# Kernel optimization log

Measured on AMD Instinct MI355X. Metric: run time of the kernel, lower is better.

The kernel has to match this reference:

```python
import jax, jax.numpy as jnp
import numpy as np

N, E, DIN, DOUT = 30000, 480000, 512, 512


def setup_inputs() -> dict:
    key = jax.random.key(0)
    ks = jax.random.split(key, 20)
    inp = {}
    inp["x"] = jax.random.normal(ks[0], (N, DIN), jnp.float32)
    inp["edge_index"] = jax.random.randint(ks[1], (2, E), 0, N, dtype=jnp.int64)
    inp["edge_weight"] = jax.random.uniform(ks[2], (E,), jnp.float32)
    sc = 1.0 / np.sqrt(DIN)
    sl = 1.0 / np.sqrt(2 * DOUT)
    for i, g in enumerate(["i", "f", "g", "o"]):
        inp[f"Wc_{g}"] = jax.random.normal(ks[3 + 4 * i], (DIN, DOUT), jnp.float32) * sc
        inp[f"bc_{g}"] = jnp.zeros((DOUT,), jnp.float32)
        inp[f"Wl_{g}"] = jax.random.normal(ks[4 + 4 * i], (2 * DOUT, DOUT), jnp.float32) * sl
        inp[f"bl_{g}"] = jnp.zeros((DOUT,), jnp.float32)
    return inp


def _gcn_norm(src, dst, w, n):
    # add self loops with weight 1.0 (improved=False), then symmetric normalization
    loops = jnp.arange(n, dtype=src.dtype)
    src = jnp.concatenate([src, loops])
    dst = jnp.concatenate([dst, loops])
    w = jnp.concatenate([w, jnp.ones((n,), w.dtype)])
    deg = jax.ops.segment_sum(w, dst, num_segments=n)
    dinv = jnp.where(deg > 0, jax.lax.rsqrt(jnp.where(deg > 0, deg, 1.0)), 0.0)
    norm = dinv[src] * w * dinv[dst]
    return src, dst, norm


def reference(x, edge_index, edge_weight,
              Wc_i, bc_i, Wl_i, bl_i,
              Wc_f, bc_f, Wl_f, bl_f,
              Wc_g, bc_g, Wl_g, bl_g,
              Wc_o, bc_o, Wl_o, bl_o):
    n = x.shape[0]
    src, dst, norm = _gcn_norm(edge_index[0], edge_index[1], edge_weight, n)
    H = jnp.zeros((n, DOUT), x.dtype)  # _set_hidden_state default
    C = jnp.zeros((n, DOUT), x.dtype)  # _set_cell_state default

    def conv(Wc, bc):
        xw = x @ Wc                                        # [N, DOUT] dense GEMM
        agg = jax.ops.segment_sum(norm[:, None] * xw[src], dst, num_segments=n)
        return agg + bc

    def gate(Wc, bc, Wl, bl, act):
        z = jnp.concatenate([conv(Wc, bc), H], axis=1)      # [N, 2*DOUT]
        return act(z @ Wl + bl)

    I = gate(Wc_i, bc_i, Wl_i, bl_i, jax.nn.sigmoid)
    F = gate(Wc_f, bc_f, Wl_f, bl_f, jax.nn.sigmoid)
    G = gate(Wc_g, bc_g, Wl_g, bl_g, jnp.tanh)
    O = gate(Wc_o, bc_o, Wl_o, bl_o, jax.nn.sigmoid)
    Cn = F * C + I * G
    Hn = O * jnp.tanh(Cn)
    return O, Hn, Cn
```

## Files before the change

### kernel.cpp

```cpp
#include <hip/hip_runtime.h>
#include <stdint.h>

typedef __bf16 bf16;
typedef __attribute__((ext_vector_type(4))) float f4;
typedef __attribute__((ext_vector_type(4))) float f32x4;
typedef __attribute__((ext_vector_type(8))) __bf16 bf8v;
typedef __attribute__((ext_vector_type(4))) __bf16 bf4v;

#define NN 30000
#define MPAD 30080
#define OUTSTRIDE 15360000
#define XB 7500
#define SC_B 1875
#define TWO32 4294967296.0

typedef __attribute__((address_space(3))) unsigned int as3_u32;
typedef __attribute__((address_space(1))) unsigned int as1_u32;

__device__ __forceinline__ void gl_lds16(const void* g, void* l) {
  __builtin_amdgcn_global_load_lds((as1_u32*)g, (as3_u32*)l, 16, 0, 0);
}

__global__ void k_xp(const float* __restrict__ x, bf16* __restrict__ xbf,
                     const int* __restrict__ ei, const float* __restrict__ ew,
                     double* __restrict__ degcnt, int E) {
  int b = blockIdx.x;
  if (b < XB) {
    int i = b * 256 + threadIdx.x;
    const f4* x4 = (const f4*)x;
    f4 a = x4[2 * i], c = x4[2 * i + 1];
    bf8v o;
#pragma unroll
    for (int j = 0; j < 4; ++j) { o[j] = (bf16)a[j]; o[4 + j] = (bf16)c[j]; }
    ((bf8v*)xbf)[i] = o;
  } else {
    int e = (b - XB) * 256 + threadIdx.x;
    if (e < E) {
      int d = ei[E + e];
      atomicAdd(&degcnt[d], (double)ew[e] + TWO32);
    }
  }
}

__global__ void k_doffs(const double* __restrict__ degcnt, float* __restrict__ dinv,
                        int* __restrict__ gctr, int2* __restrict__ off2, int n) {
  int i = blockIdx.x * 256 + threadIdx.x;
  if (i >= n) return;
  double v = degcnt[i];
  double c = (double)(long long)(v * (1.0 / TWO32));
  int cnt = (int)c;
  float deg = (float)(v - c * TWO32);
  dinv[i] = rsqrtf(deg + 1.0f);
  int start = atomicAdd(gctr, cnt);
  off2[i] = make_int2(start, start + cnt);
}

__global__ void k_fused(const int* __restrict__ ei, const float* __restrict__ ew,
                        const float* __restrict__ dinv, const int2* __restrict__ off2,
                        int* __restrict__ cursor, int2* __restrict__ sn, int E,
                        const float* __restrict__ WcA, const float* __restrict__ WlA,
                        const float* __restrict__ WcB, const float* __restrict__ WlB,
                        const float* __restrict__ WcC, const float* __restrict__ WlC,
                        bf16* __restrict__ Wt,
                        const float* __restrict__ bcA, const float* __restrict__ blA,
                        const float* __restrict__ bcB, const float* __restrict__ blB,
                        const float* __restrict__ bcC, const float* __restrict__ blC,
                        float* __restrict__ bcomb) {
  __shared__ float sWc[64][17];
  __shared__ float sWl[16][64];
  __shared__ float smr[4][64];
  int b = blockIdx.x;
  if (b < SC_B) {
    int e = b * 256 + threadIdx.x;
    if (e >= E) return;
    int s = ei[e], d = ei[E + e];
    int pos = off2[d].x + atomicAdd(&cursor[d], 1);
    sn[pos] = make_int2(s, __float_as_int(dinv[s] * ew[e] * dinv[d]));
  } else if (b < SC_B + 192) {
    int bb = b - SC_B;
    int g = bb >> 6, rem = bb & 63;
    const float* Wc; const float* Wl;
    if (g == 0)      { Wc = WcA; Wl = WlA; }
    else if (g == 1) { Wc = WcB; Wl = WlB; }
    else             { Wc = WcC; Wl = WlC; }
    int k0 = (rem & 7) * 64, j0 = (rem >> 3) * 64;
    int t = threadIdx.x, tx = t & 15, ty = t >> 4;
    float acc[4][4] = {};
    for (int c0 = 0; c0 < 512; c0 += 16) {
      { int kk = t >> 2, c4 = (t & 3) * 4;
        f4 v = *(const f4*)(Wc + (size_t)(k0 + kk) * 512 + c0 + c4);
#pragma unroll
        for (int j = 0; j < 4; ++j) sWc[kk][c4 + j] = v[j]; }
      { int cc = t >> 4, j4 = (t & 15) * 4;
        f4 v = *(const f4*)(Wl + (size_t)(c0 + cc) * 512 + j0 + j4);
        *(f4*)&sWl[cc][j4] = v; }
      __syncthreads();
#pragma unroll
      for (int cc = 0; cc < 16; ++cc) {
        float wcv[4], wlv[4];
#pragma unroll
        for (int q = 0; q < 4; ++q) wcv[q] = sWc[tx * 4 + q][cc];
#pragma unroll
        for (int a = 0; a < 4; ++a) wlv[a] = sWl[cc][ty * 4 + a];
#pragma unroll
        for (int a = 0; a < 4; ++a)
#pragma unroll
          for (int q = 0; q < 4; ++q) acc[a][q] += wlv[a] * wcv[q];
      }
      __syncthreads();
    }
#pragma unroll
    for (int a = 0; a < 4; ++a) {
      bf4v o;
#pragma unroll
      for (int q = 0; q < 4; ++q) o[q] = (bf16)acc[a][q];
      *(bf4v*)&Wt[((size_t)g * 512 + j0 + ty * 4 + a) * 512 + k0 + tx * 4] = o;
    }
  } else {
    int bb = b - SC_B - 192;
    int g = bb >> 3, jc = bb & 7;
    const float* bc; const float* bl; const float* Wl;
    if (g == 0)      { bc = bcA; bl = blA; Wl = WlA; }
    else if (g == 1) { bc = bcB; bl = blB; Wl = WlB; }
    else             { bc = bcC; bl = blC; Wl = WlC; }
    int jl = threadIdx.x & 63, part = threadIdx.x >> 6;
    int j = jc * 64 + jl;
    float s = 0.f;
    for (int c = part * 128; c < part * 128 + 128; ++c)
      s += bc[c] * Wl[(size_t)c * 512 + j];
    smr[part][jl] = s;
    __syncthreads();
    if (part == 0)
      bcomb[g * 512 + j] = bl[j] + smr[0][jl] + smr[1][jl] + smr[2][jl] + smr[3][jl];
  }
}

__global__ __launch_bounds__(256) void k_agg(const int2* __restrict__ off2, const int2* __restrict__ sn,
                                             const float* __restrict__ dinv, const bf16* __restrict__ xbf,
                                             bf16* __restrict__ ybf) {
  int wv = (blockIdx.x * 256 + threadIdx.x) >> 6;
  int lane = threadIdx.x & 63;
  if (wv >= MPAD) return;
  bf16* yrow = ybf + ((size_t)wv << 9) + lane * 8;
  if (wv >= NN) {
    bf8v z;
#pragma unroll
    for (int j = 0; j < 8; ++j) z[j] = (bf16)0.f;
    *(bf8v*)yrow = z;
    return;
  }
  float acc[8];
  float s0 = dinv[wv]; s0 *= s0;
  bf8v xv0 = *(const bf8v*)(xbf + ((size_t)wv << 9) + lane * 8);
#pragma unroll
  for (int j = 0; j < 8; ++j) acc[j] = s0 * (float)xv0[j];
  int2 seg = off2[wv];
  int e = seg.x, end = seg.y;
  int2 p0, p1, p2, p3;
  const bool have = (e + 4 <= end);
  if (have) { p0 = sn[e]; p1 = sn[e + 1]; p2 = sn[e + 2]; p3 = sn[e + 3]; }
  for (; e + 8 <= end; e += 4) {
    int2 q0 = sn[e + 4], q1 = sn[e + 5], q2 = sn[e + 6], q3 = sn[e + 7];
    bf8v v0 = *(const bf8v*)(xbf + ((size_t)p0.x << 9) + lane * 8);
    bf8v v1 = *(const bf8v*)(xbf + ((size_t)p1.x << 9) + lane * 8);
    bf8v v2 = *(const bf8v*)(xbf + ((size_t)p2.x << 9) + lane * 8);
    bf8v v3 = *(const bf8v*)(xbf + ((size_t)p3.x << 9) + lane * 8);
    float n0 = __int_as_float(p0.y), n1 = __int_as_float(p1.y);
    float n2 = __int_as_float(p2.y), n3 = __int_as_float(p3.y);
#pragma unroll
    for (int j = 0; j < 8; ++j)
      acc[j] += n0 * (float)v0[j] + n1 * (float)v1[j] + n2 * (float)v2[j] + n3 * (float)v3[j];
    p0 = q0; p1 = q1; p2 = q2; p3 = q3;
  }
  if (have) {
    bf8v v0 = *(const bf8v*)(xbf + ((size_t)p0.x << 9) + lane * 8);
    bf8v v1 = *(const bf8v*)(xbf + ((size_t)p1.x << 9) + lane * 8);
    bf8v v2 = *(const bf8v*)(xbf + ((size_t)p2.x << 9) + lane * 8);
    bf8v v3 = *(const bf8v*)(xbf + ((size_t)p3.x << 9) + lane * 8);
    float n0 = __int_as_float(p0.y), n1 = __int_as_float(p1.y);
    float n2 = __int_as_float(p2.y), n3 = __int_as_float(p3.y);
#pragma unroll
    for (int j = 0; j < 8; ++j)
      acc[j] += n0 * (float)v0[j] + n1 * (float)v1[j] + n2 * (float)v2[j] + n3 * (float)v3[j];
    e += 4;
  }
  for (; e < end; ++e) {
    int2 p = sn[e];
    bf8v v = *(const bf8v*)(xbf + ((size_t)p.x << 9) + lane * 8);
    float nn = __int_as_float(p.y);
#pragma unroll
    for (int j = 0; j < 8; ++j) acc[j] += nn * (float)v[j];
  }
  bf8v o;
#pragma unroll
  for (int j = 0; j < 8; ++j) o[j] = (bf16)acc[j];
  *(bf8v*)yrow = o;
}

__global__ __launch_bounds__(256, 5) void k_gemm(const bf16* __restrict__ A, const bf16* __restrict__ Bt,
                                                 const float* __restrict__ bcomb, float* __restrict__ out) {
  __shared__ __align__(16) char lds[32768];
  const int t = threadIdx.x, lane = t & 63, w = t >> 6;
  const int wm = w >> 1, wn = w & 1;
  const int d = blockIdx.x;
  const int s = (d & 7) * 470 + (d >> 3);
  const int m0 = (s >> 3) * 64, n0 = (s & 7) * 64;
  const int l15 = lane & 15, lhi = lane >> 4;
  f32x4 acc[3][2][2] = {};

  const int lq = lane >> 2;
  const int sw = (lane >> 3) & 3;
  const int kcol = 16 * ((lane & 3) ^ sw);
  const int rswz = 16 * (lhi ^ ((l15 >> 1) & 3));

  const char* aS = (const char*)A + ((size_t)(m0 + w * 16 + lq) << 10) + kcol;
  const char* bS[3];
#pragma unroll
  for (int i = 0; i < 3; ++i) {
    int bi = i * 4 + w, g = bi >> 2, q = bi & 3;
    bS[i] = (const char*)Bt + ((size_t)(g * 512 + n0 + q * 16 + lq) << 10) + kcol;
  }
  const int vA = (wm * 32 + l15) * 64 + rswz;
  const int vB = 4096 + (wn * 32 + l15) * 64 + rswz;

  auto stage = [&](int bufoff, int kp) {
    gl_lds16(aS + kp * 64, lds + bufoff + w * 1024 + lane * 16);
#pragma unroll
    for (int i = 0; i < 3; ++i)
      gl_lds16(bS[i] + kp * 64, lds + bufoff + 4096 + (i * 4 + w) * 1024 + lane * 16);
  };

  auto compute = [&](int bufoff) {
    bf8v af[2];
#pragma unroll
    for (int mi = 0; mi < 2; ++mi)
      af[mi] = *(const bf8v*)(lds + bufoff + vA + mi * 1024);
#pragma unroll
    for (int g = 0; g < 3; ++g) {
      bf8v b0 = *(const bf8v*)(lds + bufoff + vB + g * 4096);
      bf8v b1 = *(const bf8v*)(lds + bufoff + vB + g * 4096 + 1024);
#pragma unroll
      for (int mi = 0; mi < 2; ++mi) {
        acc[g][mi][0] = __builtin_amdgcn_mfma_f32_16x16x32_bf16(b0, af[mi], acc[g][mi][0], 0, 0, 0);
        acc[g][mi][1] = __builtin_amdgcn_mfma_f32_16x16x32_bf16(b1, af[mi], acc[g][mi][1], 0, 0, 0);
      }
    }
  };

  stage(0, 0);
  stage(16384, 1);
#pragma unroll
  for (int kp = 0; kp < 16; ++kp) {
    if (kp < 15) asm volatile("s_waitcnt vmcnt(4)" ::: "memory");
    else         asm volatile("s_waitcnt vmcnt(0)" ::: "memory");
    __builtin_amdgcn_sched_barrier(0);
    __builtin_amdgcn_s_barrier();
    __builtin_amdgcn_sched_barrier(0);
    compute((kp & 1) * 16384);
    __builtin_amdgcn_sched_barrier(0);
    __builtin_amdgcn_s_barrier();
    __builtin_amdgcn_sched_barrier(0);
    if (kp < 14) stage((kp & 1) * 16384, kp + 2);
  }

#pragma unroll
  for (int ni = 0; ni < 2; ++ni) {
    int nb = n0 + wn * 32 + ni * 16 + lhi * 4;
    f4 bI = *(const f4*)&bcomb[nb];
    f4 bG = *(const f4*)&bcomb[512 + nb];
    f4 bO = *(const f4*)&bcomb[1024 + nb];
#pragma unroll
    for (int mi = 0; mi < 2; ++mi) {
      int row = m0 + wm * 32 + mi * 16 + l15;
      if (row < NN) {
        f4 vO, vH, vC;
#pragma unroll
        for (int r = 0; r < 4; ++r) {
          float zi = acc[0][mi][ni][r] + bI[r];
          float zg = acc[1][mi][ni][r] + bG[r];
          float zo = acc[2][mi][ni][r] + bO[r];
          float I = 1.f / (1.f + __expf(-zi));
          float e2g = __expf(2.f * zg);
          float G = (e2g - 1.f) / (e2g + 1.f);
          float O = 1.f / (1.f + __expf(-zo));
          float Cn = I * G;
          float e2c = __expf(2.f * Cn);
          float tc = (e2c - 1.f) / (e2c + 1.f);
          vO[r] = O; vH[r] = O * tc; vC[r] = Cn;
        }
        size_t base = ((size_t)row << 9) + nb;
        __builtin_nontemporal_store(vO, (f4*)&out[base]);
        __builtin_nontemporal_store(vH, (f4*)&out[OUTSTRIDE + base]);
        __builtin_nontemporal_store(vC, (f4*)&out[2 * OUTSTRIDE + base]);
      }
    }
  }
}

extern "C" void kernel_launch(void* const* d_in, const int* in_sizes, int n_in,
                              void* d_out, int out_size, void* d_ws, size_t ws_size,
                              hipStream_t stream) {
  const float* x   = (const float*)d_in[0];
  const int*   ei  = (const int*)d_in[1];
  const float* ew  = (const float*)d_in[2];
  const float* Wc_i = (const float*)d_in[3];
  const float* bc_i = (const float*)d_in[4];
  const float* Wl_i = (const float*)d_in[5];
  const float* bl_i = (const float*)d_in[6];
  const float* Wc_g = (const float*)d_in[11];
  const float* bc_g = (const float*)d_in[12];
  const float* Wl_g = (const float*)d_in[13];
  const float* bl_g = (const float*)d_in[14];
  const float* Wc_o = (const float*)d_in[15];
  const float* bc_o = (const float*)d_in[16];
  const float* Wl_o = (const float*)d_in[17];
  const float* bl_o = (const float*)d_in[18];

  const int E = in_sizes[2];
  const int n = in_sizes[0] / 512;
  const int NB = (n + 255) / 256;

  char* ws = (char*)d_ws;
  bf16*  ybf   = (bf16*)ws;
  float* dinv  = (float*)(ws + 30801920);
  bf16*  Wt    = (bf16*)(ws + 30924800);
  float* bcomb = (float*)(ws + 32497664);
  (void)ws_size;

  char* ob = (char*)d_out;
  float*  out    = (float*)d_out;
  bf16*   xbf    = (bf16*)ob;
  int2*   sn     = (int2*)(ob + 30720000);
  double* degcnt = (double*)(ob + 34560000);
  int*    curs   = (int*)(ob + 34800000);
  int*    gctr   = (int*)(ob + 34920000);
  int2*   off2   = (int2*)(ob + 34920064);
  (void)out_size; (void)n_in;

  hipMemsetAsync(degcnt, 0, 360064, stream);
  k_xp<<<XB + (E + 255) / 256, 256, 0, stream>>>(x, xbf, ei, ew, degcnt, E);
  k_doffs<<<NB, 256, 0, stream>>>(degcnt, dinv, gctr, off2, n);
  k_fused<<<SC_B + 192 + 24, 256, 0, stream>>>(ei, ew, dinv, off2, curs, sn, E,
                                               Wc_i, Wl_i, Wc_g, Wl_g, Wc_o, Wl_o, Wt,
                                               bc_i, bl_i, bc_g, bl_g, bc_o, bl_o, bcomb);
  k_agg<<<(MPAD * 64 + 255) / 256, 256, 0, stream>>>(off2, sn, dinv, xbf, ybf);
  k_gemm<<<3760, 256, 0, stream>>>(ybf, Wt, bcomb, out);
}
```

Measured before the change: 279.1 us.

## Slice features into column panels for cache-local gather, pack edge metadata

Stores bf16 node features and aggregated outputs as 8 column slices of 64 values, so each aggregation pass gathers from a small, cache-resident slice. Each wave processes 8 edges at once, with groups of 8 lanes covering the slice, and combines the partial sums with cross-lane shuffles. Edge metadata is packed into 32 bits: a 16-bit source index plus a bf16-rounded norm. The GEMM A-tile loads are remapped to the sliced layout. The risks are reduced norm precision, a node-count limit of 65536, and shuffle reduction overhead.

```diff
diff --git a/kernel.cpp b/kernel.cpp
--- a/kernel.cpp
+++ b/kernel.cpp
@@ -13,6 +13,8 @@
 #define XB 7500
 #define SC_B 1875
 #define TWO32 4294967296.0
+#define SLE 1925120
+#define SLB 3850240
 
 typedef __attribute__((address_space(3))) unsigned int as3_u32;
 typedef __attribute__((address_space(1))) unsigned int as1_u32;
@@ -21,18 +23,20 @@
   __builtin_amdgcn_global_load_lds((as1_u32*)g, (as3_u32*)l, 16, 0, 0);
 }
 
-__global__ void k_xp(const float* __restrict__ x, bf16* __restrict__ xbf,
+__global__ void k_xp(const float* __restrict__ x, bf16* __restrict__ xs,
                      const int* __restrict__ ei, const float* __restrict__ ew,
                      double* __restrict__ degcnt, int E) {
   int b = blockIdx.x;
   if (b < XB) {
     int i = b * 256 + threadIdx.x;
+    int node = i >> 6, chunk = i & 63;
+    int slice = chunk >> 3, sub = chunk & 7;
     const f4* x4 = (const f4*)x;
     f4 a = x4[2 * i], c = x4[2 * i + 1];
     bf8v o;
 #pragma unroll
     for (int j = 0; j < 4; ++j) { o[j] = (bf16)a[j]; o[4 + j] = (bf16)c[j]; }
-    ((bf8v*)xbf)[i] = o;
+    *(bf8v*)(xs + (size_t)slice * SLE + (size_t)node * 64 + sub * 8) = o;
   } else {
     int e = (b - XB) * 256 + threadIdx.x;
     if (e < E) {
@@ -57,7 +61,7 @@
 
 __global__ void k_fused(const int* __restrict__ ei, const float* __restrict__ ew,
                         const float* __restrict__ dinv, const int2* __restrict__ off2,
-                        int* __restrict__ cursor, int2* __restrict__ sn, int E,
+                        int* __restrict__ cursor, unsigned* __restrict__ sn1, int E,
                         const float* __restrict__ WcA, const float* __restrict__ WlA,
                         const float* __restrict__ WcB, const float* __restrict__ WlB,
                         const float* __restrict__ WcC, const float* __restrict__ WlC,
@@ -75,7 +79,8 @@
     if (e >= E) return;
     int s = ei[e], d = ei[E + e];
     int pos = off2[d].x + atomicAdd(&cursor[d], 1);
-    sn[pos] = make_int2(s, __float_as_int(dinv[s] * ew[e] * dinv[d]));
+    float nrm = dinv[s] * ew[e] * dinv[d];
+    sn1[pos] = ((__float_as_uint(nrm) + 0x8000u) & 0xFFFF0000u) | (unsigned)s;
   } else if (b < SC_B + 192) {
     int bb = b - SC_B;
     int g = bb >> 6, rem = bb & 63;
@@ -135,66 +140,47 @@
   }
 }
 
-__global__ __launch_bounds__(256) void k_agg(const int2* __restrict__ off2, const int2* __restrict__ sn,
-                                             const float* __restrict__ dinv, const bf16* __restrict__ xbf,
-                                             bf16* __restrict__ ybf) {
-  int wv = (blockIdx.x * 256 + threadIdx.x) >> 6;
-  int lane = threadIdx.x & 63;
-  if (wv >= MPAD) return;
-  bf16* yrow = ybf + ((size_t)wv << 9) + lane * 8;
+__global__ __launch_bounds__(256) void k_agg(const int2* __restrict__ off2, const unsigned* __restrict__ sn1,
+                                             const float* __restrict__ dinv, const bf16* __restrict__ xs,
+                                             bf16* __restrict__ ys) {
+  const int slice = blockIdx.x & 7;
+  const int wv = (((blockIdx.x >> 3) << 8) + threadIdx.x) >> 6;
+  const int lane = threadIdx.x & 63;
+  const int g = lane >> 3, jc = lane & 7;
+  const bf16* xsl = xs + (size_t)slice * SLE;
+  bf16* yrow = ys + (size_t)slice * SLE + (size_t)wv * 64 + jc * 8;
   if (wv >= NN) {
-    bf8v z;
-#pragma unroll
-    for (int j = 0; j < 8; ++j) z[j] = (bf16)0.f;
-    *(bf8v*)yrow = z;
+    if (g == 0) {
+      bf8v z;
+#pragma unroll
+      for (int j = 0; j < 8; ++j) z[j] = (bf16)0.f;
+      __builtin_nontemporal_store(z, (bf8v*)yrow);
+    }
     return;
   }
-  float acc[8];
-  float s0 = dinv[wv]; s0 *= s0;
-  bf8v xv0 = *(const bf8v*)(xbf + ((size_t)wv << 9) + lane * 8);
-#pragma unroll
-  for (int j = 0; j < 8; ++j) acc[j] = s0 * (float)xv0[j];
+  float acc[8] = {};
   int2 seg = off2[wv];
-  int e = seg.x, end = seg.y;
-  int2 p0, p1, p2, p3;
-  const bool have = (e + 4 <= end);
-  if (have) { p0 = sn[e]; p1 = sn[e + 1]; p2 = sn[e + 2]; p3 = sn[e + 3]; }
-  for (; e + 8 <= end; e += 4) {
-    int2 q0 = sn[e + 4], q1 = sn[e + 5], q2 = sn[e + 6], q3 = sn[e + 7];
-    bf8v v0 = *(const bf8v*)(xbf + ((size_t)p0.x << 9) + lane * 8);
-    bf8v v1 = *(const bf8v*)(xbf + ((size_t)p1.x << 9) + lane * 8);
-    bf8v v2 = *(const bf8v*)(xbf + ((size_t)p2.x << 9) + lane * 8);
-    bf8v v3 = *(const bf8v*)(xbf + ((size_t)p3.x << 9) + lane * 8);
-    float n0 = __int_as_float(p0.y), n1 = __int_as_float(p1.y);
-    float n2 = __int_as_float(p2.y), n3 = __int_as_float(p3.y);
-#pragma unroll
-    for (int j = 0; j < 8; ++j)
-      acc[j] += n0 * (float)v0[j] + n1 * (float)v1[j] + n2 * (float)v2[j] + n3 * (float)v3[j];
-    p0 = q0; p1 = q1; p2 = q2; p3 = q3;
-  }
-  if (have) {
-    bf8v v0 = *(const bf8v*)(xbf + ((size_t)p0.x << 9) + lane * 8);
-    bf8v v1 = *(const bf8v*)(xbf + ((size_t)p1.x << 9) + lane * 8);
-    bf8v v2 = *(const bf8v*)(xbf + ((size_t)p2.x << 9) + lane * 8);
-    bf8v v3 = *(const bf8v*)(xbf + ((size_t)p3.x << 9) + lane * 8);
-    float n0 = __int_as_float(p0.y), n1 = __int_as_float(p1.y);
-    float n2 = __int_as_float(p2.y), n3 = __int_as_float(p3.y);
-#pragma unroll
-    for (int j = 0; j < 8; ++j)
-      acc[j] += n0 * (float)v0[j] + n1 * (float)v1[j] + n2 * (float)v2[j] + n3 * (float)v3[j];
-    e += 4;
-  }
-  for (; e < end; ++e) {
-    int2 p = sn[e];
-    bf8v v = *(const bf8v*)(xbf + ((size_t)p.x << 9) + lane * 8);
-    float nn = __int_as_float(p.y);
-#pragma unroll
-    for (int j = 0; j < 8; ++j) acc[j] += nn * (float)v[j];
-  }
-  bf8v o;
-#pragma unroll
-  for (int j = 0; j < 8; ++j) o[j] = (bf16)acc[j];
-  *(bf8v*)yrow = o;
+  for (int e = seg.x; e < seg.y; e += 8) {
+    int ee = e + g;
+    unsigned meta = (ee < seg.y) ? __builtin_nontemporal_load(sn1 + ee) : 0u;
+    float nrm = __uint_as_float(meta & 0xFFFF0000u);
+    int src = (int)(meta & 0xFFFFu);
+    bf8v v = *(const bf8v*)(xsl + (size_t)src * 64 + jc * 8);
+#pragma unroll
+    for (int j = 0; j < 8; ++j) acc[j] += nrm * (float)v[j];
+  }
+#pragma unroll
+  for (int m = 8; m < 64; m <<= 1)
+#pragma unroll
+    for (int j = 0; j < 8; ++j) acc[j] += __shfl_xor(acc[j], m);
+  if (g == 0) {
+    float s0 = dinv[wv]; s0 *= s0;
+    bf8v xv = *(const bf8v*)(xsl + (size_t)wv * 64 + jc * 8);
+    bf8v o;
+#pragma unroll
+    for (int j = 0; j < 8; ++j) o[j] = (bf16)(acc[j] + s0 * (float)xv[j]);
+    __builtin_nontemporal_store(o, (bf8v*)yrow);
+  }
 }
 
 __global__ __launch_bounds__(256, 5) void k_gemm(const bf16* __restrict__ A, const bf16* __restrict__ Bt,
@@ -213,7 +199,7 @@
   const int kcol = 16 * ((lane & 3) ^ sw);
   const int rswz = 16 * (lhi ^ ((l15 >> 1) & 3));
 
-  const char* aS = (const char*)A + ((size_t)(m0 + w * 16 + lq) << 10) + kcol;
+  const char* aB = (const char*)A + ((size_t)(m0 + w * 16 + lq) << 7) + kcol;
   const char* bS[3];
 #pragma unroll
   for (int i = 0; i < 3; ++i) {
@@ -224,7 +210,7 @@
   const int vB = 4096 + (wn * 32 + l15) * 64 + rswz;
 
   auto stage = [&](int bufoff, int kp) {
-    gl_lds16(aS + kp * 64, lds + bufoff + w * 1024 + lane * 16);
+    gl_lds16(aB + (size_t)(kp >> 1) * SLB + (kp & 1) * 64, lds + bufoff + w * 1024 + lane * 16);
 #pragma unroll
     for (int i = 0; i < 3; ++i)
       gl_lds16(bS[i] + kp * 64, lds + bufoff + 4096 + (i * 4 + w) * 1024 + lane * 16);
@@ -321,28 +307,28 @@
   const int NB = (n + 255) / 256;
 
   char* ws = (char*)d_ws;
-  bf16*  ybf   = (bf16*)ws;
+  bf16*  ys    = (bf16*)ws;
   float* dinv  = (float*)(ws + 30801920);
   bf16*  Wt    = (bf16*)(ws + 30924800);
   float* bcomb = (float*)(ws + 32497664);
   (void)ws_size;
 
   char* ob = (char*)d_out;
-  float*  out    = (float*)d_out;
-  bf16*   xbf    = (bf16*)ob;
-  int2*   sn     = (int2*)(ob + 30720000);
-  double* degcnt = (double*)(ob + 34560000);
-  int*    curs   = (int*)(ob + 34800000);
-  int*    gctr   = (int*)(ob + 34920000);
-  int2*   off2   = (int2*)(ob + 34920064);
+  float*    out    = (float*)d_out;
+  bf16*     xs     = (bf16*)ob;
+  unsigned* sn1    = (unsigned*)(ob + 30801920);
+  double*   degcnt = (double*)(ob + 32721920);
+  int*      curs   = (int*)(ob + 32961920);
+  int*      gctr   = (int*)(ob + 33081920);
+  int2*     off2   = (int2*)(ob + 33081984);
   (void)out_size; (void)n_in;
 
   hipMemsetAsync(degcnt, 0, 360064, stream);
-  k_xp<<<XB + (E + 255) / 256, 256, 0, stream>>>(x, xbf, ei, ew, degcnt, E);
+  k_xp<<<XB + (E + 255) / 256, 256, 0, stream>>>(x, xs, ei, ew, degcnt, E);
   k_doffs<<<NB, 256, 0, stream>>>(degcnt, dinv, gctr, off2, n);
-  k_fused<<<SC_B + 192 + 24, 256, 0, stream>>>(ei, ew, dinv, off2, curs, sn, E,
+  k_fused<<<SC_B + 192 + 24, 256, 0, stream>>>(ei, ew, dinv, off2, curs, sn1, E,
                                                Wc_i, Wl_i, Wc_g, Wl_g, Wc_o, Wl_o, Wt,
                                                bc_i, bl_i, bc_g, bl_g, bc_o, bl_o, bcomb);
-  k_agg<<<(MPAD * 64 + 255) / 256, 256, 0, stream>>>(off2, sn, dinv, xbf, ybf);
-  k_gemm<<<3760, 256, 0, stream>>>(ybf, Wt, bcomb, out);
-}
+  k_agg<<<8 * (MPAD / 4), 256, 0, stream>>>(off2, sn1, dinv, xs, ys);
+  k_gemm<<<3760, 256, 0, stream>>>(ys, Wt, bcomb, out);
+}
```

Result: slower. 347.5 us (+24.5%).
